# Kernel tuning notes

Hardware: AMD Instinct MI355X
Metric: run time of the kernel (lower is better)

Reference implementation:

```python
import jax, jax.numpy as jnp
import numpy as np

D_MODEL = 1024
NHEAD = 16
D_K = D_MODEL // NHEAD


def setup_inputs() -> dict:
    key = jax.random.key(0)
    ks = jax.random.split(key, 12)
    B, L = 4, 2048
    s = 1.0 / np.sqrt(D_MODEL)
    inp = {
        "query": jax.random.normal(ks[0], (B, L, D_MODEL), jnp.float32),
        "key": jax.random.normal(ks[1], (B, L, D_MODEL), jnp.float32),
        "value": jax.random.normal(ks[2], (B, L, D_MODEL), jnp.float32),
        "Wq": jax.random.normal(ks[3], (D_MODEL, D_MODEL), jnp.float32) * s,
        "bq": jnp.zeros((D_MODEL,), jnp.float32),
        "Wk": jax.random.normal(ks[4], (D_MODEL, D_MODEL), jnp.float32) * s,
        "bk": jnp.zeros((D_MODEL,), jnp.float32),
        "Wv": jax.random.normal(ks[5], (D_MODEL, D_MODEL), jnp.float32) * s,
        "bv": jnp.zeros((D_MODEL,), jnp.float32),
        "Wo": jax.random.normal(ks[6], (D_MODEL, D_MODEL), jnp.float32) * s,
        "bo": jnp.zeros((D_MODEL,), jnp.float32),
    }
    return inp


def reference(query, key, value, Wq, bq, Wk, bk, Wv, bv, Wo, bo):
    B, Lq, _ = query.shape
    Lk = key.shape[1]
    # Linear projections, split into heads: [B, H, L, d_k]
    Q = (query @ Wq + bq).reshape(B, Lq, NHEAD, D_K).transpose(0, 2, 1, 3)
    K = (key @ Wk + bk).reshape(B, Lk, NHEAD, D_K).transpose(0, 2, 1, 3)
    V = (value @ Wv + bv).reshape(B, Lk, NHEAD, D_K).transpose(0, 2, 1, 3)
    scale = 1.0 / jnp.sqrt(jnp.asarray(D_K, Q.dtype))
    scores = jnp.einsum("bhqd,bhkd->bhqk", Q, K) * scale  # [B,H,Lq,Lk]
    attn = jax.nn.softmax(scores, axis=-1)
    context = jnp.einsum("bhqk,bhkd->bhqd", attn, V)
    context = context.transpose(0, 2, 1, 3).reshape(B, Lq, D_MODEL)
    return context @ Wo + bo
```

## Files before the change

kernel.cpp:

```cpp
#include <hip/hip_runtime.h>
#include <hip/hip_bf16.h>
#include <cstdint>
#include <cstddef>


typedef unsigned short u16;
typedef __bf16 bf8v __attribute__((ext_vector_type(8)));
typedef __bf16 bf4v __attribute__((ext_vector_type(4)));
typedef float f32x4 __attribute__((ext_vector_type(4)));

#define D_MODEL 1024
#define NHEAD   16
#define DK      64
#define BATCH   4
#define SEQ     2048
#define ROWS    (BATCH * SEQ)

__device__ __forceinline__ u16 f2b(float f) {
  union { float f; unsigned int i; } x; x.f = f;
  unsigned int r = x.i + 0x7fffu + ((x.i >> 16) & 1u);
  return (u16)(r >> 16);
}
__device__ __forceinline__ ushort4 pack4(float a, float b, float c, float d) {
  union { bf4v v; ushort4 u; } x;
  x.v[0] = (__bf16)a; x.v[1] = (__bf16)b; x.v[2] = (__bf16)c; x.v[3] = (__bf16)d;
  return x.u;
}
__device__ __forceinline__ void async16(const void* g, void* l) {
  __builtin_amdgcn_global_load_lds((const __attribute__((address_space(1))) void*)g,
                                   (__attribute__((address_space(3))) void*)l, 16, 0, 0);
}
#define MFMA16(a, b, c) __builtin_amdgcn_mfma_f32_16x16x32_bf16(a, b, c, 0, 0, 0)

__global__ void wtrans_cvt_kernel(const float* __restrict__ w0, const float* __restrict__ w1,
                                  const float* __restrict__ w2, const float* __restrict__ w3,
                                  u16* __restrict__ dst4) {
  __shared__ float t[32][33];
  const float* src = (blockIdx.z == 0) ? w0 : (blockIdx.z == 1) ? w1
                   : (blockIdx.z == 2) ? w2 : w3;
  u16* dst = dst4 + (size_t)blockIdx.z * D_MODEL * D_MODEL;
  const int c0 = blockIdx.x * 32, r0 = blockIdx.y * 32;
  for (int i = threadIdx.y; i < 32; i += 8)
    t[i][threadIdx.x] = src[(size_t)(r0 + i) * D_MODEL + c0 + threadIdx.x];
  __syncthreads();
  for (int i = threadIdx.y; i < 32; i += 8)
    dst[(size_t)(c0 + i) * D_MODEL + r0 + threadIdx.x] = f2b(t[threadIdx.x][i]);
}

__global__ __launch_bounds__(256) void cvt_f2b_kernel(const float* __restrict__ src,
                                                      u16* __restrict__ dst, int n4) {
  const int i = blockIdx.x * 256 + threadIdx.x;
  if (i < n4) {
    const float4 v = ((const float4*)src)[i];
    ushort4 o;
    o.x = f2b(v.x); o.y = f2b(v.y); o.z = f2b(v.z); o.w = f2b(v.w);
    ((ushort4*)dst)[i] = o;
  }
}

#define BM 128
#define BN 128
#define BK 32

__global__ __launch_bounds__(256) void gemm_bt(const u16* __restrict__ A,
                                               const u16* __restrict__ Bt,
                                               const float* __restrict__ bias,
                                               void* __restrict__ out, int mode,
                                               float oscale) {
  __shared__ __align__(16) u16 As[BM * BK];
  __shared__ __align__(16) u16 Bs[BN * BK];
  const int tid = threadIdx.x;
  const int lane = tid & 63, wave = tid >> 6;
  const int wm = wave >> 1, wn = wave & 1;
  const int quad = lane >> 4, l16 = lane & 15;
  const int m0 = blockIdx.x * BM, n0 = blockIdx.y * BN;
  const int K = 1024;

  f32x4 acc[4][4];
#pragma unroll
  for (int i = 0; i < 4; i++)
#pragma unroll
    for (int j = 0; j < 4; j++) acc[i][j] = (f32x4){0.f, 0.f, 0.f, 0.f};

  const int srow = tid >> 2;
  const int sch = ((tid & 3) ^ ((tid >> 3) & 3)) * 8;
  const int fsw = (quad ^ ((l16 >> 1) & 3)) * 8;
  const u16* Ag = A + (size_t)(m0 + srow) * K + sch;
  const u16* Bg = Bt + (size_t)(n0 + srow) * K + sch;

  for (int k0 = 0; k0 < K; k0 += BK) {
    async16(Ag + k0, &As[tid * 8]);
    async16(Ag + (size_t)64 * K + k0, &As[2048 + tid * 8]);
    async16(Bg + k0, &Bs[tid * 8]);
    async16(Bg + (size_t)64 * K + k0, &Bs[2048 + tid * 8]);
    __syncthreads();

    bf8v af[4], bfr[4];
#pragma unroll
    for (int i = 0; i < 4; i++)
      af[i] = *(const bf8v*)&As[(wm * 64 + i * 16 + l16) * BK + fsw];
#pragma unroll
    for (int j = 0; j < 4; j++)
      bfr[j] = *(const bf8v*)&Bs[(wn * 64 + j * 16 + l16) * BK + fsw];
#pragma unroll
    for (int i = 0; i < 4; i++)
#pragma unroll
      for (int j = 0; j < 4; j++)
        acc[i][j] = MFMA16(af[i], bfr[j], acc[i][j]);
    __syncthreads();
  }

#pragma unroll
  for (int j = 0; j < 4; j++) {
    const int n = n0 + wn * 64 + j * 16 + l16;
    const float bv = bias[n];
#pragma unroll
    for (int i = 0; i < 4; i++) {
      const int gr0 = m0 + wm * 64 + i * 16 + quad * 4;
#pragma unroll
      for (int r = 0; r < 4; r++) {
        const int row = gr0 + r;
        const float val = (acc[i][j][r] + bv) * oscale;
        if (mode == 2) {
          ((float*)out)[(size_t)row * D_MODEL + n] = val;
        } else {
          const int b = row >> 11, l = row & 2047;
          const int h = n >> 6, d = n & 63;
          if (mode == 0)
            ((u16*)out)[(((size_t)(b * NHEAD + h) * SEQ + l) << 6) + d] = f2b(val);
          else
            ((u16*)out)[(((size_t)(b * NHEAD + h) * DK + d) << 11) + l] = f2b(val);
        }
      }
    }
  }
}

__global__ __launch_bounds__(256, 3) void attn_kernel(const u16* __restrict__ Q,
                                                      const u16* __restrict__ K,
                                                      const u16* __restrict__ Vt,
                                                      u16* __restrict__ ctx) {
  const int bh = blockIdx.y;
  const int qb = blockIdx.x * 128;
  const int tid = threadIdx.x;
  const int lane = tid & 63, wave = tid >> 6;
  const int quad = lane >> 4, l16 = lane & 15;
  const u16* Qh = Q + (size_t)bh * SEQ * DK;
  const u16* Kh = K + (size_t)bh * SEQ * DK;
  const u16* Vh = Vt + (size_t)bh * DK * SEQ;

  __shared__ __align__(16) u16 Ks[2][2][64 * 32];
  __shared__ __align__(16) u16 Vs[2][2][64 * 32];
  __shared__ __align__(16) u16 Ps[4][32 * 64];

  const int srow = tid >> 2;
  const int sch  = ((tid & 3) ^ ((tid >> 3) & 3)) * 8;
  const int ldst = tid * 8;
  const int fsw  = (quad ^ ((l16 >> 1) & 3)) * 8;

  bf8v qf[2][2];
#pragma unroll
  for (int qg = 0; qg < 2; qg++)
#pragma unroll
    for (int h = 0; h < 2; h++)
      qf[qg][h] = *(const bf8v*)&Qh[(size_t)(qb + wave * 32 + qg * 16 + l16) * DK + h * 32 + quad * 8];

  f32x4 o[2][4];
  float m_q[2], l_q[2];
#pragma unroll
  for (int qg = 0; qg < 2; qg++) {
    m_q[qg] = -1e30f; l_q[qg] = 0.f;
#pragma unroll
    for (int d = 0; d < 4; d++) o[qg][d] = (f32x4){0.f, 0.f, 0.f, 0.f};
  }

  async16(Kh + (size_t)srow * DK + sch,       &Ks[0][0][ldst]);
  async16(Kh + (size_t)srow * DK + 32 + sch,  &Ks[0][1][ldst]);
  async16(Vh + (size_t)srow * SEQ + sch,      &Vs[0][0][ldst]);
  async16(Vh + (size_t)srow * SEQ + 32 + sch, &Vs[0][1][ldst]);
  __syncthreads();

  int p = 0;
  for (int kt = 0; kt < SEQ; kt += 64) {
    const int nt = kt + 64;
    if (nt < SEQ) {
      async16(Kh + (size_t)(nt + srow) * DK + sch,      &Ks[p ^ 1][0][ldst]);
      async16(Kh + (size_t)(nt + srow) * DK + 32 + sch, &Ks[p ^ 1][1][ldst]);
      async16(Vh + (size_t)srow * SEQ + nt + sch,       &Vs[p ^ 1][0][ldst]);
      async16(Vh + (size_t)srow * SEQ + nt + 32 + sch,  &Vs[p ^ 1][1][ldst]);
    }

    bf8v kf[4][2];
#pragma unroll
    for (int nb = 0; nb < 4; nb++)
#pragma unroll
      for (int h = 0; h < 2; h++)
        kf[nb][h] = *(const bf8v*)&Ks[p][h][(nb * 16 + l16) * 32 + fsw];

#pragma unroll
    for (int qg = 0; qg < 2; qg++) {
      f32x4 s[4];
#pragma unroll
      for (int nb = 0; nb < 4; nb++) {
        f32x4 t = (f32x4){0.f, 0.f, 0.f, 0.f};
        t = MFMA16(kf[nb][0], qf[qg][0], t);
        t = MFMA16(kf[nb][1], qf[qg][1], t);
        s[nb] = t;
      }
      float mx = s[0][0];
#pragma unroll
      for (int nb = 0; nb < 4; nb++)
#pragma unroll
        for (int r = 0; r < 4; r++) mx = fmaxf(mx, s[nb][r]);
      mx = fmaxf(mx, __shfl_xor(mx, 16));
      mx = fmaxf(mx, __shfl_xor(mx, 32));
      const float Mn = fmaxf(m_q[qg], mx);
      const float al = __builtin_amdgcn_exp2f(m_q[qg] - Mn);
      m_q[qg] = Mn;
      float rs = 0.f;
#pragma unroll
      for (int nb = 0; nb < 4; nb++)
#pragma unroll
        for (int r = 0; r < 4; r++) {
          const float pv = __builtin_amdgcn_exp2f(s[nb][r] - Mn);
          s[nb][r] = pv;
          rs += pv;
        }
      rs += __shfl_xor(rs, 16);
      rs += __shfl_xor(rs, 32);
      l_q[qg] = l_q[qg] * al + rs;
#pragma unroll
      for (int d = 0; d < 4; d++) o[qg][d] *= al;

      const int prow = (wave * 32 + qg * 16 + l16) * 64;
#pragma unroll
      for (int nb = 0; nb < 4; nb++) {
        const int cp = (nb * 2 + (quad >> 1)) ^ (l16 & 7);
        *(ushort4*)&Ps[0][prow + cp * 8 + (quad & 1) * 4] =
            pack4(s[nb][0], s[nb][1], s[nb][2], s[nb][3]);
      }
    }

    bf8v vf[4][2], pf[2][2];
#pragma unroll
    for (int dc = 0; dc < 4; dc++)
#pragma unroll
      for (int kc = 0; kc < 2; kc++)
        vf[dc][kc] = *(const bf8v*)&Vs[p][kc][(dc * 16 + l16) * 32 + fsw];
#pragma unroll
    for (int qg = 0; qg < 2; qg++)
#pragma unroll
      for (int kc = 0; kc < 2; kc++)
        pf[qg][kc] = *(const bf8v*)&Ps[0][(wave * 32 + qg * 16 + l16) * 64 +
                                         (((kc * 4 + quad) ^ (l16 & 7)) * 8)];
#pragma unroll
    for (int qg = 0; qg < 2; qg++)
#pragma unroll
      for (int dc = 0; dc < 4; dc++) {
        o[qg][dc] = MFMA16(vf[dc][0], pf[qg][0], o[qg][dc]);
        o[qg][dc] = MFMA16(vf[dc][1], pf[qg][1], o[qg][dc]);
      }

    __syncthreads();
    p ^= 1;
  }

  const int b = bh >> 4, hh = bh & 15;
#pragma unroll
  for (int qg = 0; qg < 2; qg++) {
    const float inv = __builtin_amdgcn_rcpf(l_q[qg]);
    const int q = qb + wave * 32 + qg * 16 + l16;
#pragma unroll
    for (int dc = 0; dc < 4; dc++) {
      const int col = hh * 64 + dc * 16 + quad * 4;
      *(ushort4*)&ctx[(size_t)(b * SEQ + q) * D_MODEL + col] =
          pack4(o[qg][dc][0] * inv, o[qg][dc][1] * inv,
                o[qg][dc][2] * inv, o[qg][dc][3] * inv);
    }
  }
}

extern "C" void kernel_launch(void* const* d_in, const int* in_sizes, int n_in,
                              void* d_out, int out_size, void* d_ws, size_t ws_size,
                              hipStream_t stream) {
  const float* q  = (const float*)d_in[0];
  const float* k  = (const float*)d_in[1];
  const float* v  = (const float*)d_in[2];
  const float* Wq = (const float*)d_in[3];
  const float* bq = (const float*)d_in[4];
  const float* Wk = (const float*)d_in[5];
  const float* bk = (const float*)d_in[6];
  const float* Wv = (const float*)d_in[7];
  const float* bv = (const float*)d_in[8];
  const float* Wo = (const float*)d_in[9];
  const float* bo = (const float*)d_in[10];

  u16* ws  = (u16*)d_ws;
  u16* wt  = ws;
  u16* act = wt + (size_t)4 * D_MODEL * D_MODEL;
  u16* Qw  = act + (size_t)ROWS * D_MODEL;
  u16* Kw  = Qw + (size_t)ROWS * D_MODEL;
  u16* Vt  = Kw + (size_t)ROWS * D_MODEL;

  const int n4 = ROWS * D_MODEL / 4;
  dim3 gg(ROWS / BM, D_MODEL / BN), gb(256);
  const float QSCALE = 0.18033688011112042f;

  wtrans_cvt_kernel<<<dim3(32, 32, 4), dim3(32, 8), 0, stream>>>(Wq, Wk, Wv, Wo, wt);

  cvt_f2b_kernel<<<n4 / 256, 256, 0, stream>>>(q, act, n4);
  gemm_bt<<<gg, gb, 0, stream>>>(act, wt,                                 bq, Qw, 0, QSCALE);
  cvt_f2b_kernel<<<n4 / 256, 256, 0, stream>>>(k, act, n4);
  gemm_bt<<<gg, gb, 0, stream>>>(act, wt + (size_t)1 * D_MODEL * D_MODEL, bk, Kw, 0, 1.0f);
  cvt_f2b_kernel<<<n4 / 256, 256, 0, stream>>>(v, act, n4);
  gemm_bt<<<gg, gb, 0, stream>>>(act, wt + (size_t)2 * D_MODEL * D_MODEL, bv, Vt, 1, 1.0f);

  attn_kernel<<<dim3(SEQ / 128, BATCH * NHEAD), 256, 0, stream>>>(Qw, Kw, Vt, act);

  gemm_bt<<<gg, gb, 0, stream>>>(act, wt + (size_t)3 * D_MODEL * D_MODEL, bo, d_out, 2, 1.0f);
}
```

Before: 401.7 us.

## Keep P in registers, add lazy softmax rescale and MFMA priority hints

Drops the LDS staging buffer for the probability tile and builds the PV MFMA operands straight from score registers. V fragments are now read as two 4-element halves with a permuted offset so their k-order matches the register-resident P layout. Online-softmax rescaling of O and l is skipped unless some row's max grows by more than 8 (log2 units), and s_setprio brackets the MFMA sections. Occupancy hint is raised from 3 to 4 blocks per CU, which lowers the register budget and risks spills. The lazy rescale lets exp2 values exceed 1 by up to 2^8 before bf16 conversion, relying on fp32 accumulation headroom.

```diff
diff --git a/kernel.cpp b/kernel.cpp
--- a/kernel.cpp
+++ b/kernel.cpp
@@ -136,7 +136,7 @@
   }
 }
 
-__global__ __launch_bounds__(256, 3) void attn_kernel(const u16* __restrict__ Q,
+__global__ __launch_bounds__(256, 4) void attn_kernel(const u16* __restrict__ Q,
                                                       const u16* __restrict__ K,
                                                       const u16* __restrict__ Vt,
                                                       u16* __restrict__ ctx) {
@@ -151,12 +151,12 @@
 
   __shared__ __align__(16) u16 Ks[2][2][64 * 32];
   __shared__ __align__(16) u16 Vs[2][2][64 * 32];
-  __shared__ __align__(16) u16 Ps[4][32 * 64];
 
   const int srow = tid >> 2;
   const int sch  = ((tid & 3) ^ ((tid >> 3) & 3)) * 8;
   const int ldst = tid * 8;
   const int fsw  = (quad ^ ((l16 >> 1) & 3)) * 8;
+  const int voff = (((quad >> 1) ^ ((l16 >> 1) & 3)) * 8) + (quad & 1) * 4;
 
   bf8v qf[2][2];
 #pragma unroll
@@ -197,9 +197,11 @@
       for (int h = 0; h < 2; h++)
         kf[nb][h] = *(const bf8v*)&Ks[p][h][(nb * 16 + l16) * 32 + fsw];
 
+    bf8v pf[2][2];
 #pragma unroll
     for (int qg = 0; qg < 2; qg++) {
       f32x4 s[4];
+      __builtin_amdgcn_s_setprio(1);
 #pragma unroll
       for (int nb = 0; nb < 4; nb++) {
         f32x4 t = (f32x4){0.f, 0.f, 0.f, 0.f};
@@ -207,16 +209,22 @@
         t = MFMA16(kf[nb][1], qf[qg][1], t);
         s[nb] = t;
       }
-      float mx = s[0][0];
-#pragma unroll
-      for (int nb = 0; nb < 4; nb++)
-#pragma unroll
-        for (int r = 0; r < 4; r++) mx = fmaxf(mx, s[nb][r]);
+      __builtin_amdgcn_s_setprio(0);
+      float t0 = fmaxf(fmaxf(s[0][0], s[0][1]), fmaxf(s[0][2], s[0][3]));
+      float t1 = fmaxf(fmaxf(s[1][0], s[1][1]), fmaxf(s[1][2], s[1][3]));
+      float t2 = fmaxf(fmaxf(s[2][0], s[2][1]), fmaxf(s[2][2], s[2][3]));
+      float t3 = fmaxf(fmaxf(s[3][0], s[3][1]), fmaxf(s[3][2], s[3][3]));
+      float mx = fmaxf(fmaxf(t0, t1), fmaxf(t2, t3));
       mx = fmaxf(mx, __shfl_xor(mx, 16));
       mx = fmaxf(mx, __shfl_xor(mx, 32));
-      const float Mn = fmaxf(m_q[qg], mx);
-      const float al = __builtin_amdgcn_exp2f(m_q[qg] - Mn);
-      m_q[qg] = Mn;
+      const float mprev = m_q[qg];
+      float Mn = mprev, al = 1.f;
+      const int resc = !__all(mx - mprev <= 8.0f);
+      if (resc) {
+        Mn = fmaxf(mprev, mx);
+        al = __builtin_amdgcn_exp2f(mprev - Mn);
+        m_q[qg] = Mn;
+      }
       float rs = 0.f;
 #pragma unroll
       for (int nb = 0; nb < 4; nb++)
@@ -228,31 +236,37 @@
         }
       rs += __shfl_xor(rs, 16);
       rs += __shfl_xor(rs, 32);
-      l_q[qg] = l_q[qg] * al + rs;
-#pragma unroll
-      for (int d = 0; d < 4; d++) o[qg][d] *= al;
-
-      const int prow = (wave * 32 + qg * 16 + l16) * 64;
-#pragma unroll
-      for (int nb = 0; nb < 4; nb++) {
-        const int cp = (nb * 2 + (quad >> 1)) ^ (l16 & 7);
-        *(ushort4*)&Ps[0][prow + cp * 8 + (quad & 1) * 4] =
-            pack4(s[nb][0], s[nb][1], s[nb][2], s[nb][3]);
-      }
-    }
-
-    bf8v vf[4][2], pf[2][2];
-#pragma unroll
-    for (int dc = 0; dc < 4; dc++)
-#pragma unroll
-      for (int kc = 0; kc < 2; kc++)
-        vf[dc][kc] = *(const bf8v*)&Vs[p][kc][(dc * 16 + l16) * 32 + fsw];
-#pragma unroll
-    for (int qg = 0; qg < 2; qg++)
-#pragma unroll
-      for (int kc = 0; kc < 2; kc++)
-        pf[qg][kc] = *(const bf8v*)&Ps[0][(wave * 32 + qg * 16 + l16) * 64 +
-                                         (((kc * 4 + quad) ^ (l16 & 7)) * 8)];
+      if (resc) {
+        l_q[qg] = l_q[qg] * al + rs;
+#pragma unroll
+        for (int d = 0; d < 4; d++) o[qg][d] *= al;
+      } else {
+        l_q[qg] += rs;
+      }
+#pragma unroll
+      for (int kc = 0; kc < 2; kc++) {
+        bf8v pw;
+#pragma unroll
+        for (int j = 0; j < 4; j++) {
+          pw[j]     = (__bf16)s[2 * kc][j];
+          pw[j + 4] = (__bf16)s[2 * kc + 1][j];
+        }
+        pf[qg][kc] = pw;
+      }
+    }
+
+    bf8v vf[4][2];
+#pragma unroll
+    for (int dc = 0; dc < 4; dc++) {
+      const int rb = (dc * 16 + l16) * 32 + voff;
+#pragma unroll
+      for (int kc = 0; kc < 2; kc++) {
+        const bf4v lo = *(const bf4v*)&Vs[p][kc][rb];
+        const bf4v hi = *(const bf4v*)&Vs[p][kc][rb ^ 16];
+        vf[dc][kc] = __builtin_shufflevector(lo, hi, 0, 1, 2, 3, 4, 5, 6, 7);
+      }
+    }
+    __builtin_amdgcn_s_setprio(1);
 #pragma unroll
     for (int qg = 0; qg < 2; qg++)
 #pragma unroll
@@ -260,6 +274,7 @@
         o[qg][dc] = MFMA16(vf[dc][0], pf[qg][0], o[qg][dc]);
         o[qg][dc] = MFMA16(vf[dc][1], pf[qg][1], o[qg][dc]);
       }
+    __builtin_amdgcn_s_setprio(0);
 
     __syncthreads();
     p ^= 1;
```

Result: no change. 398.1 us (-0.9%).
